# Performance work log

Hardware: AMD Instinct MI355X
Metric: run time of the kernel (lower is better)

The kernel has to match this reference:

```python
import jax, jax.numpy as jnp
import numpy as np

D_MODEL = 1024
N_HEADS = 16
D_K = D_MODEL // N_HEADS
THETA = 10000.0
NEG_INF = -1e30


def _rope_tables(token_positions, d_k, theta=THETA):
    # freqs[t, i] = t / theta**(2i/d_k), i in [0, d_k/2)
    exponent = jnp.arange(0, d_k, 2, dtype=jnp.float32)  # [d_k/2]
    inv_freq = 1.0 / theta ** (exponent / d_k)
    freqs = token_positions.astype(jnp.float32)[:, None] * inv_freq[None, :]  # [s, d_k/2]
    return jnp.cos(freqs), jnp.sin(freqs)


def _apply_rope(x, cos, sin):
    # x: [..., s, d_k]; interleaved pair rotation (pairs are (x[2i], x[2i+1]))
    x1 = x[..., 0::2]
    x2 = x[..., 1::2]
    r1 = x1 * cos - x2 * sin
    r2 = x1 * sin + x2 * cos
    return jnp.stack([r1, r2], axis=-1).reshape(x.shape)


def setup_inputs() -> dict:
    key = jax.random.key(0)
    ks = jax.random.split(key, 5)
    b, s = 2, 2048
    scale = np.sqrt(2.0 / (D_MODEL + D_MODEL))
    return {
        "x": jax.random.normal(ks[0], (b, s, D_MODEL), dtype=jnp.float32),
        "Wq": jax.random.normal(ks[1], (D_MODEL, D_MODEL), dtype=jnp.float32) * scale,
        "Wk": jax.random.normal(ks[2], (D_MODEL, D_MODEL), dtype=jnp.float32) * scale,
        "Wv": jax.random.normal(ks[3], (D_MODEL, D_MODEL), dtype=jnp.float32) * scale,
        "Wo": jax.random.normal(ks[4], (D_MODEL, D_MODEL), dtype=jnp.float32) * scale,
        "token_positions": jnp.arange(s, dtype=jnp.int64 if jax.config.jax_enable_x64 else jnp.int32),
    }


def reference(x, Wq, Wk, Wv, Wo, token_positions):
    b, s, _ = x.shape
    # QKV projections: weight stored [in, out]
    q = jnp.einsum('bsi,io->bso', x, Wq)
    k = jnp.einsum('bsi,io->bso', x, Wk)
    v = jnp.einsum('bsi,io->bso', x, Wv)
    # split heads: [b, h, s, d_k]
    q = q.reshape(b, s, N_HEADS, D_K).transpose(0, 2, 1, 3)
    k = k.reshape(b, s, N_HEADS, D_K).transpose(0, 2, 1, 3)
    v = v.reshape(b, s, N_HEADS, D_K).transpose(0, 2, 1, 3)
    # RoPE
    cos, sin = _rope_tables(token_positions, D_K)
    q = _apply_rope(q, cos, sin)
    k = _apply_rope(k, cos, sin)
    # causal attention with full materialized scores (faithful to source)
    scores = jnp.einsum('bhid,bhjd->bhij', q, k) / jnp.sqrt(jnp.float32(D_K))
    mask = jnp.tril(jnp.ones((s, s), dtype=bool))
    scores = jnp.where(mask, scores, NEG_INF)
    probs = jax.nn.softmax(scores, axis=-1)
    out = jnp.einsum('bhij,bhjd->bhid', probs, v)
    out = out.transpose(0, 2, 1, 3).reshape(b, s, D_MODEL)
    return jnp.einsum('bsi,io->bso', out, Wo)
```

## Files before the change

### kernel.cpp

```cpp
#include <hip/hip_runtime.h>
#include <cmath>

#define S_LEN 2048
#define DMODEL 1024
#define NHEADS 16
#define DK 64
#define BATCH 2
#define MTOT (BATCH * S_LEN)

using short8 = __attribute__((ext_vector_type(8))) short;
using floatx4 = __attribute__((ext_vector_type(4))) float;

__device__ __forceinline__ unsigned short f2b(float f) {
    union { float f; unsigned u; } v; v.f = f;
    unsigned r = v.u + 0x7fff + ((v.u >> 16) & 1);
    return (unsigned short)(r >> 16);
}

__device__ __forceinline__ void gload16(const void* g, void* l) {
    __builtin_amdgcn_global_load_lds(
        (const __attribute__((address_space(1))) unsigned int*)g,
        (__attribute__((address_space(3))) unsigned int*)l, 16, 0, 0);
}

__global__ __launch_bounds__(256) void prep_k(
    const float* __restrict__ x, unsigned short* __restrict__ xb,
    const int* __restrict__ tokpos, float* __restrict__ ct, float* __restrict__ st,
    const float* W0, const float* W1, const float* W2, const float* W3,
    unsigned short* T0, unsigned short* T1, unsigned short* T2, unsigned short* T3) {
    __shared__ float t[64][65];
    const int b = blockIdx.x;
    if (b < 2048) {
        int i = (b * 256 + threadIdx.x) * 8;
        float4 a = *(const float4*)(x + i);
        float4 bb = *(const float4*)(x + i + 4);
        short8 o;
        o[0] = f2b(a.x); o[1] = f2b(a.y); o[2] = f2b(a.z); o[3] = f2b(a.w);
        o[4] = f2b(bb.x); o[5] = f2b(bb.y); o[6] = f2b(bb.z); o[7] = f2b(bb.w);
        *(short8*)(xb + i) = o;
    } else if (b < 2304) {
        int idx = (b - 2048) * 256 + threadIdx.x;
        int si = idx >> 5;
        int ip = idx & 31;
        float pos = (float)tokpos[si];
        float inv_freq = powf(10000.0f, -(float)(2 * ip) / 64.0f);
        float ang = pos * inv_freq;
        ct[idx] = cosf(ang);
        st[idx] = sinf(ang);
    } else {
        int id = b - 2304;
        int z = id >> 8;
        int bx = id & 15, by = (id >> 4) & 15;
        const float* W = z == 0 ? W0 : z == 1 ? W1 : z == 2 ? W2 : W3;
        unsigned short* T = z == 0 ? T0 : z == 1 ? T1 : z == 2 ? T2 : T3;
        const bool perm = (z < 2);
        int n0 = bx * 64, k0 = by * 64;
        int rr = threadIdx.x >> 6, cc = threadIdx.x & 63;
#pragma unroll
        for (int r = 0; r < 16; r++) {
            int row = r * 4 + rr;
            t[row][cc] = W[(size_t)(k0 + row) * DMODEL + n0 + cc];
        }
        __syncthreads();
#pragma unroll
        for (int r = 0; r < 16; r++) {
            int row = r * 4 + rr;
            int drow = perm ? (((row & 1) ? 32 : 0) + (row >> 1)) : row;
            T[(size_t)(n0 + drow) * DMODEL + k0 + cc] = f2b(t[cc][row]);
        }
    }
}

__global__ __launch_bounds__(256) void vtrans_k(const unsigned short* __restrict__ V,
                                                unsigned short* __restrict__ Vt) {
    __shared__ unsigned short t[64][72];
    const int tid = threadIdx.x;
    const int s0 = blockIdx.x * 64, d0 = blockIdx.y * 64;
    const int bb = s0 >> 11;
#pragma unroll
    for (int it = 0; it < 4; it++) {
        int e = (it * 256 + tid) * 4;
        int r = e >> 6, c = e & 63;
        *(ushort4*)&t[r][c] = *(const ushort4*)(V + (size_t)(s0 + r) * DMODEL + d0 + c);
    }
    __syncthreads();
#pragma unroll
    for (int it = 0; it < 4; it++) {
        int e = (it * 256 + tid) * 4;
        int r = e >> 6, c = e & 63;
        ushort4 v;
        v.x = t[c + 0][r]; v.y = t[c + 1][r];
        v.z = t[c + 2][r]; v.w = t[c + 3][r];
        *(ushort4*)(Vt + (size_t)(bb * 1024 + d0 + r) * S_LEN + (s0 & (S_LEN - 1)) + c) = v;
    }
}

__global__ __launch_bounds__(256) void mm_k(
    const unsigned short* __restrict__ A,
    const unsigned short* __restrict__ Bt0, const unsigned short* __restrict__ Bt1,
    const unsigned short* __restrict__ Bt2,
    void* C0, void* C1, void* C2,
    const float* __restrict__ ct, const float* __restrict__ st, int kind) {
    __shared__ __align__(16) unsigned short blob[8192];

    const int z = blockIdx.z;
    const unsigned short* Bt = z == 0 ? Bt0 : z == 1 ? Bt1 : Bt2;
    void* C = z == 0 ? C0 : z == 1 ? C1 : C2;
    const int mode = (kind == 1) ? 0 : (z == 2 ? 3 : 1);

    const int tid = threadIdx.x;
    const int w = tid >> 6, lane = tid & 63;
    const int l15 = lane & 15, quad = lane >> 4;
    const int wr = w >> 1, wc = w & 1;
    const int m0 = blockIdx.x * 128, n0 = blockIdx.y * 128;

    floatx4 acc[4][4];
#pragma unroll
    for (int i = 0; i < 4; i++)
#pragma unroll
        for (int j = 0; j < 4; j++) acc[i][j] = (floatx4){0.f, 0.f, 0.f, 0.f};

    for (int k0 = 0; k0 < DMODEL; k0 += 32) {
        if (k0) __syncthreads();
#pragma unroll
        for (int it = 0; it < 4; it++) {
            int g = it * 4 + w;
            const unsigned short* gp;
            if (g < 8)
                gp = A + (size_t)(m0 + g * 16 + l15) * DMODEL + k0 + (lane >> 4) * 8;
            else
                gp = Bt + (size_t)(n0 + (g - 8) * 16 + l15) * DMODEL + k0 + (lane >> 4) * 8;
            gload16(gp, (char*)blob + g * 1024);
        }
        __syncthreads();

        short8 af[4], bfr[4];
#pragma unroll
        for (int i = 0; i < 4; i++)
            af[i] = *(const short8*)((char*)blob + ((wr * 4 + i) * 64 + lane) * 16);
#pragma unroll
        for (int j = 0; j < 4; j++)
            bfr[j] = *(const short8*)((char*)blob + 8192 + ((wc * 4 + j) * 64 + lane) * 16);
#pragma unroll
        for (int i = 0; i < 4; i++)
#pragma unroll
            for (int j = 0; j < 4; j++)
                acc[i][j] = __builtin_amdgcn_mfma_f32_16x16x32_bf16(af[i], bfr[j], acc[i][j], 0, 0, 0);
    }

#pragma unroll
    for (int i = 0; i < 4; i++) {
        const int rowb = m0 + wr * 64 + i * 16 + quad * 4;
        if (mode == 0) {
            float* Cf = (float*)C;
#pragma unroll
            for (int j = 0; j < 4; j++) {
                int colb = n0 + wc * 64 + j * 16 + l15;
#pragma unroll
                for (int r = 0; r < 4; r++)
                    Cf[(size_t)(rowb + r) * DMODEL + colb] = acc[i][j][r];
            }
        } else if (mode == 1) {
            unsigned short* Cb = (unsigned short*)C;
#pragma unroll
            for (int jh = 0; jh < 2; jh++) {
                int ip = jh * 16 + l15;
                int cole = n0 + wc * 64 + jh * 16 + l15;
#pragma unroll
                for (int r = 0; r < 4; r++) {
                    int row = rowb + r;
                    int si = row & (S_LEN - 1);
                    float c = ct[si * 32 + ip];
                    float s = st[si * 32 + ip];
                    float e = acc[i][jh][r];
                    float od = acc[i][jh + 2][r];
                    Cb[(size_t)row * DMODEL + cole] = f2b(e * c - od * s);
                    Cb[(size_t)row * DMODEL + cole + 32] = f2b(e * s + od * c);
                }
            }
        } else {
            unsigned short* Cb = (unsigned short*)C;
#pragma unroll
            for (int j = 0; j < 4; j++) {
                int colb = n0 + wc * 64 + j * 16 + l15;
#pragma unroll
                for (int r = 0; r < 4; r++)
                    Cb[(size_t)(rowb + r) * DMODEL + colb] = f2b(acc[i][j][r]);
            }
        }
    }
}

__global__ __launch_bounds__(512) void attn_k(const unsigned short* __restrict__ Q,
                                              const unsigned short* __restrict__ K,
                                              const unsigned short* __restrict__ Vt,
                                              unsigned short* __restrict__ O) {
    __shared__ __align__(16) unsigned short Kblob[2][4096];
    __shared__ __align__(16) unsigned short Vblob[2][4096];
    __shared__ __align__(16) unsigned short Ps[8][16 * 72];

    const int tid = threadIdx.x;
    const int w = tid >> 6, lane = tid & 63;
    const int l15 = lane & 15, quad = lane >> 4;
    const int idx = blockIdx.x;
    const int qt = 15 - (idx >> 5);
    const int bh = idx & 31;
    const int bb = bh >> 4, h = bh & 15;
    const int qbase = qt * 128 + w * 16;
    const int qrow = qbase + l15;

    const size_t qoff = (size_t)(bb * S_LEN + qbase + l15) * DMODEL + h * DK;
    short8 aq0 = *(const short8*)(Q + qoff + quad * 8);
    short8 aq1 = *(const short8*)(Q + qoff + 32 + quad * 8);

    floatx4 o[4];
#pragma unroll
    for (int f = 0; f < 4; f++) o[f] = (floatx4){0.f, 0.f, 0.f, 0.f};
    float mv = -1e30f, lv = 0.f;

    const unsigned short* Kb = K + (size_t)(bb * S_LEN) * DMODEL + h * DK;
    const unsigned short* Vb = Vt + (size_t)(bb * 1024 + h * DK) * S_LEN;
    unsigned short* ps = &Ps[w][0];

    auto stage = [&](int b, int kb) {
#pragma unroll
        for (int it = 0; it < 2; it++) {
            int g = it * 8 + w;
            if (g < 8) {
                const unsigned short* gp =
                    Kb + (size_t)(kb + (g >> 1) * 16 + l15) * DMODEL + (g & 1) * 32 + quad * 8;
                gload16(gp, (char*)&Kblob[b][0] + g * 1024);
            } else {
                int gv = g - 8;
                const unsigned short* gp =
                    Vb + (size_t)((gv >> 1) * 16 + l15) * S_LEN + kb + (gv & 1) * 32 + quad * 8;
                gload16(gp, (char*)&Vblob[b][0] + gv * 1024);
            }
        }
    };

    const int nkt = 2 * qt + 2;
    stage(0, 0);
    for (int kt = 0; kt < nkt; kt++) {
        const int b = kt & 1;
        const int kb = kt * 64;
        __syncthreads();
        if (kt + 1 < nkt) stage(b ^ 1, (kt + 1) * 64);

        const unsigned short* kbb = &Kblob[b][0];
        floatx4 c[4];
#pragma unroll
        for (int g = 0; g < 4; g++) {
            short8 kf0 = *(const short8*)(kbb + (g * 2 + 0) * 512 + lane * 8);
            short8 kf1 = *(const short8*)(kbb + (g * 2 + 1) * 512 + lane * 8);
            floatx4 t = {0.f, 0.f, 0.f, 0.f};
            t = __builtin_amdgcn_mfma_f32_16x16x32_bf16(kf0, aq0, t, 0, 0, 0);
            c[g] = __builtin_amdgcn_mfma_f32_16x16x32_bf16(kf1, aq1, t, 0, 0, 0);
        }

        float sv[16];
#pragma unroll
        for (int g = 0; g < 4; g++)
#pragma unroll
            for (int r = 0; r < 4; r++) {
                int key = kb + g * 16 + quad * 4 + r;
                sv[g * 4 + r] = (key <= qrow) ? c[g][r] * 0.125f : -1e30f;
            }
        float mx = sv[0];
#pragma unroll
        for (int i = 1; i < 16; i++) mx = fmaxf(mx, sv[i]);
        mx = fmaxf(mx, __shfl_xor(mx, 16));
        mx = fmaxf(mx, __shfl_xor(mx, 32));
        float mnew = fmaxf(mv, mx);
        float alpha = __expf(mv - mnew);
        mv = mnew;
        float p[16], psum = 0.f;
#pragma unroll
        for (int i = 0; i < 16; i++) {
            p[i] = __expf(sv[i] - mnew);
            psum += p[i];
        }
        lv = lv * alpha + psum;

#pragma unroll
        for (int g = 0; g < 4; g++) {
            ushort4 pk;
            pk.x = f2b(p[g * 4 + 0]); pk.y = f2b(p[g * 4 + 1]);
            pk.z = f2b(p[g * 4 + 2]); pk.w = f2b(p[g * 4 + 3]);
            *(ushort4*)(ps + l15 * 72 + g * 16 + quad * 4) = pk;
        }
#pragma unroll
        for (int f = 0; f < 4; f++) {
            o[f][0] *= alpha; o[f][1] *= alpha;
            o[f][2] *= alpha; o[f][3] *= alpha;
        }
        short8 pf0 = *(const short8*)(ps + l15 * 72 + quad * 8);
        short8 pf1 = *(const short8*)(ps + l15 * 72 + 32 + quad * 8);
        const unsigned short* vbb = &Vblob[b][0];
#pragma unroll
        for (int f = 0; f < 4; f++) {
            short8 vf0 = *(const short8*)(vbb + (f * 2 + 0) * 512 + lane * 8);
            short8 vf1 = *(const short8*)(vbb + (f * 2 + 1) * 512 + lane * 8);
            o[f] = __builtin_amdgcn_mfma_f32_16x16x32_bf16(vf0, pf0, o[f], 0, 0, 0);
            o[f] = __builtin_amdgcn_mfma_f32_16x16x32_bf16(vf1, pf1, o[f], 0, 0, 0);
        }
    }

    lv += __shfl_xor(lv, 16);
    lv += __shfl_xor(lv, 32);
    float inv = 1.0f / lv;
    __syncthreads();
#pragma unroll
    for (int f = 0; f < 4; f++) {
        ushort4 pk;
        pk.x = f2b(o[f][0] * inv);
        pk.y = f2b(o[f][1] * inv);
        pk.z = f2b(o[f][2] * inv);
        pk.w = f2b(o[f][3] * inv);
        *(ushort4*)(ps + l15 * 72 + f * 16 + quad * 4) = pk;
    }
    short8 r0 = *(const short8*)(ps + l15 * 72 + quad * 8);
    short8 r1 = *(const short8*)(ps + l15 * 72 + 32 + quad * 8);
    size_t obase = (size_t)(bb * S_LEN + qbase + l15) * DMODEL + h * DK;
    *(short8*)(O + obase + quad * 8) = r0;
    *(short8*)(O + obase + 32 + quad * 8) = r1;
}

extern "C" void kernel_launch(void* const* d_in, const int* in_sizes, int n_in,
                              void* d_out, int out_size, void* d_ws,
                              size_t ws_size, hipStream_t stream) {
    const float* x = (const float*)d_in[0];
    const float* Wq = (const float*)d_in[1];
    const float* Wk = (const float*)d_in[2];
    const float* Wv = (const float*)d_in[3];
    const float* Wo = (const float*)d_in[4];
    const int* tokpos = (const int*)d_in[5];
    float* out = (float*)d_out;

    const size_t MD = (size_t)MTOT * DMODEL;
    const size_t WD = (size_t)DMODEL * DMODEL;
    unsigned short* xb = (unsigned short*)d_ws;
    unsigned short* Wqt = xb + MD;
    unsigned short* Wkt = Wqt + WD;
    unsigned short* Wvt = Wkt + WD;
    unsigned short* Wot = Wvt + WD;
    unsigned short* Q = Wot + WD;
    unsigned short* K = Q + MD;
    unsigned short* V = K + MD;
    unsigned short* Vt = V + MD;
    float* ct = (float*)(Vt + MD);
    float* st = ct + S_LEN * 32;
    unsigned short* O = V;

    prep_k<<<dim3(3328), dim3(256), 0, stream>>>(x, xb, tokpos, ct, st,
                                                 Wq, Wk, Wv, Wo, Wqt, Wkt, Wvt, Wot);

    mm_k<<<dim3(32, 8, 3), dim3(256), 0, stream>>>(xb, Wqt, Wkt, Wvt,
                                                   (void*)Q, (void*)K, (void*)V, ct, st, 0);
    vtrans_k<<<dim3(64, 16), dim3(256), 0, stream>>>(V, Vt);
    attn_k<<<dim3(512), dim3(512), 0, stream>>>(Q, K, Vt, O);
    mm_k<<<dim3(32, 8, 1), dim3(256), 0, stream>>>(O, Wot, Wot, Wot,
                                                   (void*)out, (void*)out, (void*)out, ct, st, 1);
}
```

Baseline: 218.6 us.

## Process two query sub-tiles per wave in attention and fold softmax scale into Q

The attention kernel now runs 4 waves per block, each handling 32 query rows as two 16-row sub-tiles, so every K and V fragment read from LDS feeds two MFMAs instead of one. Block size drops from 512 to 256 threads, and each wave issues more of the K/V staging loads. Separately, the 1/sqrt(d_k) scale is folded into the Q RoPE epilogue of the projection GEMM, which removes a multiply per score. The cost is higher register pressure and fewer waves per block to hide latency.

Result: slower. 226.4 us (+3.5%).

```diff
diff --git a/kernel.cpp b/kernel.cpp
--- a/kernel.cpp
+++ b/kernel.cpp
@@ -107,6 +107,7 @@
     const unsigned short* Bt = z == 0 ? Bt0 : z == 1 ? Bt1 : Bt2;
     void* C = z == 0 ? C0 : z == 1 ? C1 : C2;
     const int mode = (kind == 1) ? 0 : (z == 2 ? 3 : 1);
+    const float qscale = (z == 0) ? 0.125f : 1.0f;
 
     const int tid = threadIdx.x;
     const int w = tid >> 6, lane = tid & 63;
@@ -170,8 +171,8 @@
                 for (int r = 0; r < 4; r++) {
                     int row = rowb + r;
                     int si = row & (S_LEN - 1);
-                    float c = ct[si * 32 + ip];
-                    float s = st[si * 32 + ip];
+                    float c = ct[si * 32 + ip] * qscale;
+                    float s = st[si * 32 + ip] * qscale;
                     float e = acc[i][jh][r];
                     float od = acc[i][jh + 2][r];
                     Cb[(size_t)row * DMODEL + cole] = f2b(e * c - od * s);
@@ -191,13 +192,13 @@
     }
 }
 
-__global__ __launch_bounds__(512) void attn_k(const unsigned short* __restrict__ Q,
+__global__ __launch_bounds__(256) void attn_k(const unsigned short* __restrict__ Q,
                                               const unsigned short* __restrict__ K,
                                               const unsigned short* __restrict__ Vt,
                                               unsigned short* __restrict__ O) {
     __shared__ __align__(16) unsigned short Kblob[2][4096];
     __shared__ __align__(16) unsigned short Vblob[2][4096];
-    __shared__ __align__(16) unsigned short Ps[8][16 * 72];
+    __shared__ __align__(16) unsigned short Ps[4][32 * 72];
 
     const int tid = threadIdx.x;
     const int w = tid >> 6, lane = tid & 63;
@@ -206,17 +207,22 @@
     const int qt = 15 - (idx >> 5);
     const int bh = idx & 31;
     const int bb = bh >> 4, h = bh & 15;
-    const int qbase = qt * 128 + w * 16;
-    const int qrow = qbase + l15;
-
-    const size_t qoff = (size_t)(bb * S_LEN + qbase + l15) * DMODEL + h * DK;
-    short8 aq0 = *(const short8*)(Q + qoff + quad * 8);
-    short8 aq1 = *(const short8*)(Q + qoff + 32 + quad * 8);
-
-    floatx4 o[4];
-#pragma unroll
-    for (int f = 0; f < 4; f++) o[f] = (floatx4){0.f, 0.f, 0.f, 0.f};
-    float mv = -1e30f, lv = 0.f;
+    const int qb = qt * 128 + w * 32;
+
+    short8 aq0[2], aq1[2];
+#pragma unroll
+    for (int j = 0; j < 2; j++) {
+        const size_t qoff = (size_t)(bb * S_LEN + qb + j * 16 + l15) * DMODEL + h * DK;
+        aq0[j] = *(const short8*)(Q + qoff + quad * 8);
+        aq1[j] = *(const short8*)(Q + qoff + 32 + quad * 8);
+    }
+
+    floatx4 o[4][2];
+#pragma unroll
+    for (int f = 0; f < 4; f++)
+#pragma unroll
+        for (int j = 0; j < 2; j++) o[f][j] = (floatx4){0.f, 0.f, 0.f, 0.f};
+    float mv[2] = {-1e30f, -1e30f}, lv[2] = {0.f, 0.f};
 
     const unsigned short* Kb = K + (size_t)(bb * S_LEN) * DMODEL + h * DK;
     const unsigned short* Vb = Vt + (size_t)(bb * 1024 + h * DK) * S_LEN;
@@ -224,8 +230,8 @@
 
     auto stage = [&](int b, int kb) {
 #pragma unroll
-        for (int it = 0; it < 2; it++) {
-            int g = it * 8 + w;
+        for (int it = 0; it < 4; it++) {
+            int g = it * 4 + w;
             if (g < 8) {
                 const unsigned short* gp =
                     Kb + (size_t)(kb + (g >> 1) * 16 + l15) * DMODEL + (g & 1) * 32 + quad * 8;
@@ -248,82 +254,104 @@
         if (kt + 1 < nkt) stage(b ^ 1, (kt + 1) * 64);
 
         const unsigned short* kbb = &Kblob[b][0];
-        floatx4 c[4];
+        floatx4 c[4][2];
 #pragma unroll
         for (int g = 0; g < 4; g++) {
             short8 kf0 = *(const short8*)(kbb + (g * 2 + 0) * 512 + lane * 8);
             short8 kf1 = *(const short8*)(kbb + (g * 2 + 1) * 512 + lane * 8);
-            floatx4 t = {0.f, 0.f, 0.f, 0.f};
-            t = __builtin_amdgcn_mfma_f32_16x16x32_bf16(kf0, aq0, t, 0, 0, 0);
-            c[g] = __builtin_amdgcn_mfma_f32_16x16x32_bf16(kf1, aq1, t, 0, 0, 0);
-        }
-
-        float sv[16];
-#pragma unroll
-        for (int g = 0; g < 4; g++)
-#pragma unroll
-            for (int r = 0; r < 4; r++) {
-                int key = kb + g * 16 + quad * 4 + r;
-                sv[g * 4 + r] = (key <= qrow) ? c[g][r] * 0.125f : -1e30f;
-            }
-        float mx = sv[0];
-#pragma unroll
-        for (int i = 1; i < 16; i++) mx = fmaxf(mx, sv[i]);
-        mx = fmaxf(mx, __shfl_xor(mx, 16));
-        mx = fmaxf(mx, __shfl_xor(mx, 32));
-        float mnew = fmaxf(mv, mx);
-        float alpha = __expf(mv - mnew);
-        mv = mnew;
-        float p[16], psum = 0.f;
-#pragma unroll
-        for (int i = 0; i < 16; i++) {
-            p[i] = __expf(sv[i] - mnew);
-            psum += p[i];
-        }
-        lv = lv * alpha + psum;
-
-#pragma unroll
-        for (int g = 0; g < 4; g++) {
-            ushort4 pk;
-            pk.x = f2b(p[g * 4 + 0]); pk.y = f2b(p[g * 4 + 1]);
-            pk.z = f2b(p[g * 4 + 2]); pk.w = f2b(p[g * 4 + 3]);
-            *(ushort4*)(ps + l15 * 72 + g * 16 + quad * 4) = pk;
-        }
-#pragma unroll
-        for (int f = 0; f < 4; f++) {
-            o[f][0] *= alpha; o[f][1] *= alpha;
-            o[f][2] *= alpha; o[f][3] *= alpha;
-        }
-        short8 pf0 = *(const short8*)(ps + l15 * 72 + quad * 8);
-        short8 pf1 = *(const short8*)(ps + l15 * 72 + 32 + quad * 8);
+#pragma unroll
+            for (int j = 0; j < 2; j++) {
+                floatx4 t = {0.f, 0.f, 0.f, 0.f};
+                t = __builtin_amdgcn_mfma_f32_16x16x32_bf16(kf0, aq0[j], t, 0, 0, 0);
+                c[g][j] = __builtin_amdgcn_mfma_f32_16x16x32_bf16(kf1, aq1[j], t, 0, 0, 0);
+            }
+        }
+
+        float alpha[2];
+#pragma unroll
+        for (int j = 0; j < 2; j++) {
+            const int qrow = qb + j * 16 + l15;
+            float sv[16];
+#pragma unroll
+            for (int g = 0; g < 4; g++)
+#pragma unroll
+                for (int r = 0; r < 4; r++) {
+                    int key = kb + g * 16 + quad * 4 + r;
+                    sv[g * 4 + r] = (key <= qrow) ? c[g][j][r] : -1e30f;
+                }
+            float mx = sv[0];
+#pragma unroll
+            for (int i = 1; i < 16; i++) mx = fmaxf(mx, sv[i]);
+            mx = fmaxf(mx, __shfl_xor(mx, 16));
+            mx = fmaxf(mx, __shfl_xor(mx, 32));
+            float mnew = fmaxf(mv[j], mx);
+            alpha[j] = __expf(mv[j] - mnew);
+            mv[j] = mnew;
+            float p[16], psum = 0.f;
+#pragma unroll
+            for (int i = 0; i < 16; i++) {
+                p[i] = __expf(sv[i] - mnew);
+                psum += p[i];
+            }
+            lv[j] = lv[j] * alpha[j] + psum;
+
+#pragma unroll
+            for (int g = 0; g < 4; g++) {
+                ushort4 pk;
+                pk.x = f2b(p[g * 4 + 0]); pk.y = f2b(p[g * 4 + 1]);
+                pk.z = f2b(p[g * 4 + 2]); pk.w = f2b(p[g * 4 + 3]);
+                *(ushort4*)(ps + (j * 16 + l15) * 72 + g * 16 + quad * 4) = pk;
+            }
+        }
+#pragma unroll
+        for (int f = 0; f < 4; f++)
+#pragma unroll
+            for (int j = 0; j < 2; j++) {
+                o[f][j][0] *= alpha[j]; o[f][j][1] *= alpha[j];
+                o[f][j][2] *= alpha[j]; o[f][j][3] *= alpha[j];
+            }
+        short8 pf0[2], pf1[2];
+#pragma unroll
+        for (int j = 0; j < 2; j++) {
+            pf0[j] = *(const short8*)(ps + (j * 16 + l15) * 72 + quad * 8);
+            pf1[j] = *(const short8*)(ps + (j * 16 + l15) * 72 + 32 + quad * 8);
+        }
         const unsigned short* vbb = &Vblob[b][0];
 #pragma unroll
         for (int f = 0; f < 4; f++) {
             short8 vf0 = *(const short8*)(vbb + (f * 2 + 0) * 512 + lane * 8);
             short8 vf1 = *(const short8*)(vbb + (f * 2 + 1) * 512 + lane * 8);
-            o[f] = __builtin_amdgcn_mfma_f32_16x16x32_bf16(vf0, pf0, o[f], 0, 0, 0);
-            o[f] = __builtin_amdgcn_mfma_f32_16x16x32_bf16(vf1, pf1, o[f], 0, 0, 0);
-        }
-    }
-
-    lv += __shfl_xor(lv, 16);
-    lv += __shfl_xor(lv, 32);
-    float inv = 1.0f / lv;
-    __syncthreads();
-#pragma unroll
-    for (int f = 0; f < 4; f++) {
-        ushort4 pk;
-        pk.x = f2b(o[f][0] * inv);
-        pk.y = f2b(o[f][1] * inv);
-        pk.z = f2b(o[f][2] * inv);
-        pk.w = f2b(o[f][3] * inv);
-        *(ushort4*)(ps + l15 * 72 + f * 16 + quad * 4) = pk;
-    }
-    short8 r0 = *(const short8*)(ps + l15 * 72 + quad * 8);
-    short8 r1 = *(const short8*)(ps + l15 * 72 + 32 + quad * 8);
-    size_t obase = (size_t)(bb * S_LEN + qbase + l15) * DMODEL + h * DK;
-    *(short8*)(O + obase + quad * 8) = r0;
-    *(short8*)(O + obase + 32 + quad * 8) = r1;
+#pragma unroll
+            for (int j = 0; j < 2; j++) {
+                o[f][j] = __builtin_amdgcn_mfma_f32_16x16x32_bf16(vf0, pf0[j], o[f][j], 0, 0, 0);
+                o[f][j] = __builtin_amdgcn_mfma_f32_16x16x32_bf16(vf1, pf1[j], o[f][j], 0, 0, 0);
+            }
+        }
+    }
+
+#pragma unroll
+    for (int j = 0; j < 2; j++) {
+        lv[j] += __shfl_xor(lv[j], 16);
+        lv[j] += __shfl_xor(lv[j], 32);
+        float inv = 1.0f / lv[j];
+#pragma unroll
+        for (int f = 0; f < 4; f++) {
+            ushort4 pk;
+            pk.x = f2b(o[f][j][0] * inv);
+            pk.y = f2b(o[f][j][1] * inv);
+            pk.z = f2b(o[f][j][2] * inv);
+            pk.w = f2b(o[f][j][3] * inv);
+            *(ushort4*)(ps + (j * 16 + l15) * 72 + f * 16 + quad * 4) = pk;
+        }
+    }
+#pragma unroll
+    for (int j = 0; j < 2; j++) {
+        short8 r0 = *(const short8*)(ps + (j * 16 + l15) * 72 + quad * 8);
+        short8 r1 = *(const short8*)(ps + (j * 16 + l15) * 72 + 32 + quad * 8);
+        size_t obase = (size_t)(bb * S_LEN + qb + j * 16 + l15) * DMODEL + h * DK;
+        *(short8*)(O + obase + quad * 8) = r0;
+        *(short8*)(O + obase + 32 + quad * 8) = r1;
+    }
 }
 
 extern "C" void kernel_launch(void* const* d_in, const int* in_sizes, int n_in,
@@ -358,7 +386,7 @@
     mm_k<<<dim3(32, 8, 3), dim3(256), 0, stream>>>(xb, Wqt, Wkt, Wvt,
                                                    (void*)Q, (void*)K, (void*)V, ct, st, 0);
     vtrans_k<<<dim3(64, 16), dim3(256), 0, stream>>>(V, Vt);
-    attn_k<<<dim3(512), dim3(512), 0, stream>>>(Q, K, Vt, O);
+    attn_k<<<dim3(512), dim3(256), 0, stream>>>(Q, K, Vt, O);
     mm_k<<<dim3(32, 8, 1), dim3(256), 0, stream>>>(O, Wot, Wot, Wot,
                                                    (void*)out, (void*)out, (void*)out, ct, st, 1);
 }
```

## Fuse V transpose into projection epilogue and fold softmax scale into Q

Applied to the files above, without the earlier changes.

Removes the separate vtrans_k kernel: the V projection epilogue now transposes its tile through LDS (padded 70-wide rows) and writes V directly in [b, d, s] layout with 16-byte stores. The 1/sqrt(dk) scale moves into the Q RoPE epilogue by scaling the cos/sin factors, dropping a multiply per score in the attention inner loop. This saves one launch plus a full read and write of V. In exchange, the GEMM's LDS footprint grows slightly and Q is rounded to bf16 after scaling, a power of two.

New measurement: 228.2 us. 4.4% more time.

```diff
diff --git a/kernel.cpp b/kernel.cpp
--- a/kernel.cpp
+++ b/kernel.cpp
@@ -71,42 +71,19 @@
     }
 }
 
-__global__ __launch_bounds__(256) void vtrans_k(const unsigned short* __restrict__ V,
-                                                unsigned short* __restrict__ Vt) {
-    __shared__ unsigned short t[64][72];
-    const int tid = threadIdx.x;
-    const int s0 = blockIdx.x * 64, d0 = blockIdx.y * 64;
-    const int bb = s0 >> 11;
-#pragma unroll
-    for (int it = 0; it < 4; it++) {
-        int e = (it * 256 + tid) * 4;
-        int r = e >> 6, c = e & 63;
-        *(ushort4*)&t[r][c] = *(const ushort4*)(V + (size_t)(s0 + r) * DMODEL + d0 + c);
-    }
-    __syncthreads();
-#pragma unroll
-    for (int it = 0; it < 4; it++) {
-        int e = (it * 256 + tid) * 4;
-        int r = e >> 6, c = e & 63;
-        ushort4 v;
-        v.x = t[c + 0][r]; v.y = t[c + 1][r];
-        v.z = t[c + 2][r]; v.w = t[c + 3][r];
-        *(ushort4*)(Vt + (size_t)(bb * 1024 + d0 + r) * S_LEN + (s0 & (S_LEN - 1)) + c) = v;
-    }
-}
-
 __global__ __launch_bounds__(256) void mm_k(
     const unsigned short* __restrict__ A,
     const unsigned short* __restrict__ Bt0, const unsigned short* __restrict__ Bt1,
     const unsigned short* __restrict__ Bt2,
     void* C0, void* C1, void* C2,
     const float* __restrict__ ct, const float* __restrict__ st, int kind) {
-    __shared__ __align__(16) unsigned short blob[8192];
+    __shared__ __align__(16) unsigned short blob[8960];
 
     const int z = blockIdx.z;
     const unsigned short* Bt = z == 0 ? Bt0 : z == 1 ? Bt1 : Bt2;
     void* C = z == 0 ? C0 : z == 1 ? C1 : C2;
     const int mode = (kind == 1) ? 0 : (z == 2 ? 3 : 1);
+    const float qscale = (z == 0 && kind == 0) ? 0.125f : 1.0f;
 
     const int tid = threadIdx.x;
     const int w = tid >> 6, lane = tid & 63;
@@ -148,6 +125,43 @@
                 acc[i][j] = __builtin_amdgcn_mfma_f32_16x16x32_bf16(af[i], bfr[j], acc[i][j], 0, 0, 0);
     }
 
+    if (mode == 3) {
+        __syncthreads();
+        unsigned short* tw = blob + w * 2240;
+        unsigned short* Cb = (unsigned short*)C;
+        const int gmb = m0 + wr * 64;
+        const int bb2 = gmb >> 11;
+        const int srow0 = gmb & (S_LEN - 1);
+#pragma unroll
+        for (int jh = 0; jh < 2; jh++) {
+#pragma unroll
+            for (int jj = 0; jj < 2; jj++) {
+                int j = jh * 2 + jj;
+                int nl = jj * 16 + l15;
+#pragma unroll
+                for (int i = 0; i < 4; i++) {
+                    ushort4 pk;
+                    pk.x = f2b(acc[i][j][0]);
+                    pk.y = f2b(acc[i][j][1]);
+                    pk.z = f2b(acc[i][j][2]);
+                    pk.w = f2b(acc[i][j][3]);
+                    *(ushort4*)(tw + nl * 70 + i * 16 + quad * 4) = pk;
+                }
+            }
+            int nl = lane >> 1, mh = (lane & 1) * 32;
+            short8 q0 = *(const short8*)(tw + nl * 70 + mh + 0);
+            short8 q1 = *(const short8*)(tw + nl * 70 + mh + 8);
+            short8 q2 = *(const short8*)(tw + nl * 70 + mh + 16);
+            short8 q3 = *(const short8*)(tw + nl * 70 + mh + 24);
+            int gn = n0 + wc * 64 + jh * 32 + nl;
+            unsigned short* dst = Cb + (size_t)(bb2 * 1024 + gn) * S_LEN + srow0 + mh;
+            *(short8*)(dst + 0) = q0;
+            *(short8*)(dst + 8) = q1;
+            *(short8*)(dst + 16) = q2;
+            *(short8*)(dst + 24) = q3;
+        }
+        return;
+    }
 #pragma unroll
     for (int i = 0; i < 4; i++) {
         const int rowb = m0 + wr * 64 + i * 16 + quad * 4;
@@ -160,7 +174,7 @@
                 for (int r = 0; r < 4; r++)
                     Cf[(size_t)(rowb + r) * DMODEL + colb] = acc[i][j][r];
             }
-        } else if (mode == 1) {
+        } else {
             unsigned short* Cb = (unsigned short*)C;
 #pragma unroll
             for (int jh = 0; jh < 2; jh++) {
@@ -170,22 +184,13 @@
                 for (int r = 0; r < 4; r++) {
                     int row = rowb + r;
                     int si = row & (S_LEN - 1);
-                    float c = ct[si * 32 + ip];
-                    float s = st[si * 32 + ip];
+                    float c = ct[si * 32 + ip] * qscale;
+                    float s = st[si * 32 + ip] * qscale;
                     float e = acc[i][jh][r];
                     float od = acc[i][jh + 2][r];
                     Cb[(size_t)row * DMODEL + cole] = f2b(e * c - od * s);
                     Cb[(size_t)row * DMODEL + cole + 32] = f2b(e * s + od * c);
                 }
-            }
-        } else {
-            unsigned short* Cb = (unsigned short*)C;
-#pragma unroll
-            for (int j = 0; j < 4; j++) {
-                int colb = n0 + wc * 64 + j * 16 + l15;
-#pragma unroll
-                for (int r = 0; r < 4; r++)
-                    Cb[(size_t)(rowb + r) * DMODEL + colb] = f2b(acc[i][j][r]);
             }
         }
     }
@@ -264,7 +269,7 @@
 #pragma unroll
             for (int r = 0; r < 4; r++) {
                 int key = kb + g * 16 + quad * 4 + r;
-                sv[g * 4 + r] = (key <= qrow) ? c[g][r] * 0.125f : -1e30f;
+                sv[g * 4 + r] = (key <= qrow) ? c[g][r] : -1e30f;
             }
         float mx = sv[0];
 #pragma unroll
@@ -346,18 +351,16 @@
     unsigned short* Wot = Wvt + WD;
     unsigned short* Q = Wot + WD;
     unsigned short* K = Q + MD;
-    unsigned short* V = K + MD;
-    unsigned short* Vt = V + MD;
-    float* ct = (float*)(Vt + MD);
+    unsigned short* Vt = K + MD;
+    unsigned short* O = Vt + MD;
+    float* ct = (float*)(O + MD);
     float* st = ct + S_LEN * 32;
-    unsigned short* O = V;
 
     prep_k<<<dim3(3328), dim3(256), 0, stream>>>(x, xb, tokpos, ct, st,
                                                  Wq, Wk, Wv, Wo, Wqt, Wkt, Wvt, Wot);
 
     mm_k<<<dim3(32, 8, 3), dim3(256), 0, stream>>>(xb, Wqt, Wkt, Wvt,
-                                                   (void*)Q, (void*)K, (void*)V, ct, st, 0);
-    vtrans_k<<<dim3(64, 16), dim3(256), 0, stream>>>(V, Vt);
+                                                   (void*)Q, (void*)K, (void*)Vt, ct, st, 0);
     attn_k<<<dim3(512), dim3(512), 0, stream>>>(Q, K, Vt, O);
     mm_k<<<dim3(32, 8, 1), dim3(256), 0, stream>>>(O, Wot, Wot, Wot,
                                                    (void*)out, (void*)out, (void*)out, ct, st, 1);
```
